# Optimization experiments

Hardware: AMD Instinct MI355X
Metric: run time of the kernel (lower is better)

The kernel has to match this reference:

```python
import jax, jax.numpy as jnp
import numpy as np

N_NODES = 100000


def gcn_conv(x, W, b, src, dst, n_nodes):
    # GCNConv: h = x @ W; add self-loops; symmetric norm; aggregate; + bias
    h = x @ W  # [N, out]
    loop = jnp.arange(n_nodes, dtype=src.dtype)
    s = jnp.concatenate([src, loop])  # source of each message
    d = jnp.concatenate([dst, loop])  # target of each message
    ones = jnp.ones(d.shape[0], dtype=x.dtype)
    deg = jax.ops.segment_sum(ones, d, num_segments=n_nodes)  # in-degree incl. self-loop
    dinv = jnp.where(deg > 0, jax.lax.rsqrt(deg), 0.0)
    norm = dinv[s] * dinv[d]  # [E+N]
    msg = h[s] * norm[:, None]  # gather + scale
    out = jax.ops.segment_sum(msg, d, num_segments=n_nodes)  # scatter-add
    return out + b


def setup_inputs() -> dict:
    key = jax.random.key(0)
    k1, k2, k3, k4, k5 = jax.random.split(key, 5)
    nfeat, nhid, nclass = 128, 128, 40
    x = jax.random.normal(k1, (N_NODES, nfeat), dtype=jnp.float32)
    edge_index = jax.random.randint(k2, (2, 640000), 0, N_NODES, dtype=jnp.int64)
    # Glorot-style init for conv weights, zero bias (PyG defaults)
    W1 = jax.random.normal(k3, (nfeat, nhid), dtype=jnp.float32) * (1.0 / np.sqrt(nfeat))
    b1 = jnp.zeros((nhid,), dtype=jnp.float32)
    W2 = jax.random.normal(k4, (nhid, nclass), dtype=jnp.float32) * (1.0 / np.sqrt(nhid))
    b2 = jnp.zeros((nclass,), dtype=jnp.float32)
    return {"x": x, "edge_index": edge_index, "W1": W1, "b1": b1, "W2": W2, "b2": b2}


def reference(x, edge_index, W1, b1, W2, b2):
    src, dst = edge_index[0], edge_index[1]
    n = x.shape[0]
    # layer 1 + relu (dropout is identity at inference)
    h = gcn_conv(x, W1, b1, src, dst, n)
    h = jax.nn.relu(h)
    # final layer (no activation)
    out = gcn_conv(h, W2, b2, src, dst, n)
    return out
```

## Files before the change

kernel.cpp:

```cpp
#include <hip/hip_runtime.h>
#include <stdint.h>

#define N_NODES 100000
#define NB 782
#define NBP 784
#define BCAP 1536

typedef __attribute__((ext_vector_type(8))) short bf16x8;
typedef __attribute__((ext_vector_type(4))) float f32x4;

__device__ __forceinline__ unsigned short f2bf(float f){
    uint32_t u = __float_as_uint(f);
    uint32_t r = (u + 0x7FFFu + ((u >> 16) & 1u)) >> 16;
    return (unsigned short)r;
}
__device__ __forceinline__ float bf2f(unsigned short h){
    return __uint_as_float(((uint32_t)h) << 16);
}

__global__ void zero_u32(uint32_t* p, int n){
    int i = blockIdx.x * 256 + threadIdx.x;
    if (i < n) p[i] = 0u;
}

__global__ void to_bf16(const float* __restrict__ in, unsigned short* __restrict__ outp, int n4){
    int i = blockIdx.x * 256 + threadIdx.x;
    if (i < n4){
        float4 v = ((const float4*)in)[i];
        ushort4 o = { f2bf(v.x), f2bf(v.y), f2bf(v.z), f2bf(v.w) };
        ((ushort4*)outp)[i] = o;
    }
}

__global__ void transpose_w_frag(const float* __restrict__ W, unsigned short* __restrict__ Wtf,
                                 int NC, int total){
    int i = blockIdx.x * 256 + threadIdx.x;
    if (i < total){
        int j  = i & 7;
        int l  = (i >> 3) & 63;
        int st = (i >> 9) & 3;
        int cb = i >> 11;
        int k   = st * 32 + (l >> 4) * 8 + j;
        int col = cb * 16 + (l & 15);
        float v = (col < NC) ? W[(size_t)k * NC + col] : 0.f;
        Wtf[i] = f2bf(v);
    }
}

__global__ __launch_bounds__(1024) void bucket_hist(const int* __restrict__ dst,
        uint32_t* __restrict__ hist, int E){
    __shared__ uint32_t h[NBP];
    for (int i = threadIdx.x; i < NB; i += 1024) h[i] = 0u;
    __syncthreads();
    int base = blockIdx.x * 12800;
    for (int i = threadIdx.x; i < 12800; i += 1024){
        int e = base + i;
        if (e < E) atomicAdd(&h[(uint32_t)dst[e] >> 7], 1u);
    }
    __syncthreads();
    for (int i = threadIdx.x; i < NB; i += 1024)
        if (h[i]) atomicAdd(&hist[i], h[i]);
}

__global__ void scan_buckets(const uint32_t* __restrict__ hist,
                             uint32_t* __restrict__ base, uint32_t* __restrict__ cur){
    __shared__ uint32_t tmp[1024];
    int t = threadIdx.x;
    for (int j = t; j < 1024; j += 256) tmp[j] = (j < NB) ? hist[j] : 0u;
    __syncthreads();
    for (int off = 1; off < 1024; off <<= 1){
        uint32_t v[4];
        for (int j = 0; j < 4; j++){
            int i = t + j * 256;
            v[j] = (i >= off) ? tmp[i - off] : 0u;
        }
        __syncthreads();
        for (int j = 0; j < 4; j++) tmp[t + j * 256] += v[j];
        __syncthreads();
    }
    for (int j = t; j < NB; j += 256){
        uint32_t v = (j > 0) ? tmp[j - 1] : 0u;
        base[j] = v;
        cur[j] = v;
    }
}

__global__ __launch_bounds__(1024) void bucket_scatter(const int* __restrict__ src,
        const int* __restrict__ dst, uint32_t* __restrict__ cur,
        uint32_t* __restrict__ ebuf, int E){
    __shared__ uint32_t h[NBP];
    __shared__ uint32_t st[NBP];
    for (int i = threadIdx.x; i < NB; i += 1024) h[i] = 0u;
    __syncthreads();
    int base = blockIdx.x * 12800;
    for (int i = threadIdx.x; i < 12800; i += 1024){
        int e = base + i;
        if (e < E) atomicAdd(&h[(uint32_t)dst[e] >> 7], 1u);
    }
    __syncthreads();
    for (int i = threadIdx.x; i < NB; i += 1024){
        uint32_t c = h[i];
        st[i] = c ? atomicAdd(&cur[i], c) : 0u;
        h[i] = 0u;
    }
    __syncthreads();
    for (int i = threadIdx.x; i < 12800; i += 1024){
        int e = base + i;
        if (e < E){
            uint32_t d = (uint32_t)dst[e];
            uint32_t b = d >> 7;
            uint32_t r = atomicAdd(&h[b], 1u);
            ebuf[st[b] + r] = ((d & 127u) << 17) | (uint32_t)src[e];
        }
    }
}

__global__ __launch_bounds__(256) void bucket_csr(const uint32_t* __restrict__ hist,
        const uint32_t* __restrict__ base, const uint32_t* __restrict__ ebuf,
        uint32_t* __restrict__ offs, uint32_t* __restrict__ cnt, float* __restrict__ dinv,
        uint32_t* __restrict__ slot, int N){
    __shared__ uint32_t ebl[BCAP];
    __shared__ uint32_t ncnt[128], loff[128], ncur[128], stmp[128];
    int b = blockIdx.x, t = threadIdx.x;
    uint32_t eb = base[b], ec = hist[b];
    if (ec > BCAP) ec = BCAP;
    for (uint32_t i = t; i < ec; i += 256) ebl[i] = ebuf[eb + i];
    if (t < 128){ ncnt[t] = 0u; ncur[t] = 0u; }
    __syncthreads();
    for (uint32_t i = t; i < ec; i += 256) atomicAdd(&ncnt[ebl[i] >> 17], 1u);
    __syncthreads();
    if (t < 128) stmp[t] = ncnt[t];
    __syncthreads();
    for (int off = 1; off < 128; off <<= 1){
        uint32_t v = 0u;
        if (t < 128 && t >= off) v = stmp[t - off];
        __syncthreads();
        if (t < 128) stmp[t] += v;
        __syncthreads();
    }
    if (t < 128) loff[t] = stmp[t] - ncnt[t];
    __syncthreads();
    int g = b * 128 + t;
    if (t < 128 && g < N){
        offs[g] = eb + loff[t];
        cnt[g]  = ncnt[t];
        dinv[g] = rsqrtf((float)(ncnt[t] + 1u));
    }
    for (uint32_t i = t; i < ec; i += 256){
        uint32_t p  = ebl[i];
        uint32_t ld = p >> 17;
        uint32_t r  = atomicAdd(&ncur[ld], 1u);
        slot[eb + loff[ld] + r] = p & 0x1FFFFu;
    }
}

__global__ __launch_bounds__(256) void agg_bf(const unsigned short* __restrict__ Xh,
        const uint32_t* __restrict__ offs, const uint32_t* __restrict__ cnt,
        const uint32_t* __restrict__ slot, const float* __restrict__ dinv,
        unsigned short* __restrict__ OUT){
    int wgid = blockIdx.x * 4 + (threadIdx.x >> 6);
    int lane = threadIdx.x & 63;
    int h = lane >> 5, l = lane & 31;
    int g = wgid * 2 + h;
    const ushort4* X4 = (const ushort4*)Xh;
    uint32_t o = offs[g], c = cnt[g];
    float ax = 0.f, ay = 0.f, az = 0.f, aw = 0.f;
    #pragma unroll 1
    for (uint32_t base = 0; base < c; base += 32){
        int rem = (int)(c - base); if (rem > 32) rem = 32;
        uint32_t idx = 0u; float ds = 0.f;
        if (l < rem){
            idx = slot[o + base + (uint32_t)l];
            ds = dinv[idx];
        }
        int groups = (rem + 7) >> 3;
        #pragma unroll 1
        for (int gq = 0; gq < groups; gq++){
            int eb = gq * 8;
            ushort4 v[8]; float d[8];
            #pragma unroll
            for (int j = 0; j < 8; j++){
                uint32_t s = (uint32_t)__shfl((int)idx, eb + j, 32);
                d[j] = __shfl(ds, eb + j, 32);
                v[j] = X4[(size_t)s * 32 + l];
            }
            #pragma unroll
            for (int j = 0; j < 8; j++){
                ax += d[j] * bf2f(v[j].x);
                ay += d[j] * bf2f(v[j].y);
                az += d[j] * bf2f(v[j].z);
                aw += d[j] * bf2f(v[j].w);
            }
        }
    }
    float dd = dinv[g];
    ushort4 sv = X4[(size_t)g * 32 + l];
    ushort4 r = { f2bf(dd * (ax + dd * bf2f(sv.x))),
                  f2bf(dd * (ay + dd * bf2f(sv.y))),
                  f2bf(dd * (az + dd * bf2f(sv.z))),
                  f2bf(dd * (aw + dd * bf2f(sv.w))) };
    ((ushort4*)OUT)[(size_t)g * 32 + l] = r;
}

__global__ __launch_bounds__(256) void gemm_mfma_l1(const unsigned short* __restrict__ Xagg,
        const unsigned short* __restrict__ Wtf, const float* __restrict__ bias,
        unsigned short* __restrict__ OUT){
    int tid = threadIdx.x;
    int wid = tid >> 6, l = tid & 63;
    int lm = l & 15, lk = l >> 4;
    int rw = blockIdx.x * 64 + wid * 16;
    int ra = rw + lm; ra = ra < N_NODES ? ra : N_NODES - 1;
    const bf16x8* Wv = (const bf16x8*)Wtf;

    f32x4 acc[8] = {};
    bf16x8 aA, aB, bA[8], bB[8];

    aA = *(const bf16x8*)(Xagg + (size_t)ra * 128 + lk * 8);
    #pragma unroll
    for (int cb = 0; cb < 8; cb++) bA[cb] = Wv[(size_t)(cb * 4 + 0) * 64 + l];

    aB = *(const bf16x8*)(Xagg + (size_t)ra * 128 + 32 + lk * 8);
    #pragma unroll
    for (int cb = 0; cb < 8; cb++) bB[cb] = Wv[(size_t)(cb * 4 + 1) * 64 + l];
    #pragma unroll
    for (int cb = 0; cb < 8; cb++)
        acc[cb] = __builtin_amdgcn_mfma_f32_16x16x32_bf16(aA, bA[cb], acc[cb], 0, 0, 0);

    aA = *(const bf16x8*)(Xagg + (size_t)ra * 128 + 64 + lk * 8);
    #pragma unroll
    for (int cb = 0; cb < 8; cb++) bA[cb] = Wv[(size_t)(cb * 4 + 2) * 64 + l];
    #pragma unroll
    for (int cb = 0; cb < 8; cb++)
        acc[cb] = __builtin_amdgcn_mfma_f32_16x16x32_bf16(aB, bB[cb], acc[cb], 0, 0, 0);

    aB = *(const bf16x8*)(Xagg + (size_t)ra * 128 + 96 + lk * 8);
    #pragma unroll
    for (int cb = 0; cb < 8; cb++) bB[cb] = Wv[(size_t)(cb * 4 + 3) * 64 + l];
    #pragma unroll
    for (int cb = 0; cb < 8; cb++)
        acc[cb] = __builtin_amdgcn_mfma_f32_16x16x32_bf16(aA, bA[cb], acc[cb], 0, 0, 0);

    #pragma unroll
    for (int cb = 0; cb < 8; cb++)
        acc[cb] = __builtin_amdgcn_mfma_f32_16x16x32_bf16(aB, bB[cb], acc[cb], 0, 0, 0);

    #pragma unroll
    for (int cb = 0; cb < 8; cb++){
        int col = cb * 16 + lm;
        float bs = bias[col];
        #pragma unroll
        for (int i = 0; i < 4; i++){
            int row = rw + lk * 4 + i;
            if (row < N_NODES)
                OUT[(size_t)row * 128 + col] = f2bf(fmaxf(acc[cb][i] + bs, 0.f));
        }
    }
}

__global__ __launch_bounds__(256) void gemm_mfma_l2(const unsigned short* __restrict__ Aagg,
        const unsigned short* __restrict__ Wtf, const float* __restrict__ bias,
        float* __restrict__ OUT){
    int tid = threadIdx.x;
    int wid = tid >> 6, l = tid & 63;
    int lm = l & 15, lk = l >> 4;
    int rw = blockIdx.x * 64 + wid * 16;
    int ra = rw + lm; ra = ra < N_NODES ? ra : N_NODES - 1;
    const bf16x8* Wv = (const bf16x8*)Wtf;

    f32x4 acc[3] = {};
    bf16x8 aA, aB, bA[3], bB[3];

    aA = *(const bf16x8*)(Aagg + (size_t)ra * 128 + lk * 8);
    #pragma unroll
    for (int cb = 0; cb < 3; cb++) bA[cb] = Wv[(size_t)(cb * 4 + 0) * 64 + l];

    aB = *(const bf16x8*)(Aagg + (size_t)ra * 128 + 32 + lk * 8);
    #pragma unroll
    for (int cb = 0; cb < 3; cb++) bB[cb] = Wv[(size_t)(cb * 4 + 1) * 64 + l];
    #pragma unroll
    for (int cb = 0; cb < 3; cb++)
        acc[cb] = __builtin_amdgcn_mfma_f32_16x16x32_bf16(aA, bA[cb], acc[cb], 0, 0, 0);

    aA = *(const bf16x8*)(Aagg + (size_t)ra * 128 + 64 + lk * 8);
    #pragma unroll
    for (int cb = 0; cb < 3; cb++) bA[cb] = Wv[(size_t)(cb * 4 + 2) * 64 + l];
    #pragma unroll
    for (int cb = 0; cb < 3; cb++)
        acc[cb] = __builtin_amdgcn_mfma_f32_16x16x32_bf16(aB, bB[cb], acc[cb], 0, 0, 0);

    aB = *(const bf16x8*)(Aagg + (size_t)ra * 128 + 96 + lk * 8);
    #pragma unroll
    for (int cb = 0; cb < 3; cb++) bB[cb] = Wv[(size_t)(cb * 4 + 3) * 64 + l];
    #pragma unroll
    for (int cb = 0; cb < 3; cb++)
        acc[cb] = __builtin_amdgcn_mfma_f32_16x16x32_bf16(aA, bA[cb], acc[cb], 0, 0, 0);

    #pragma unroll
    for (int cb = 0; cb < 3; cb++)
        acc[cb] = __builtin_amdgcn_mfma_f32_16x16x32_bf16(aB, bB[cb], acc[cb], 0, 0, 0);

    #pragma unroll
    for (int cb = 0; cb < 3; cb++){
        int col = cb * 16 + lm;
        if (col < 40){
            float bs = bias[col];
            #pragma unroll
            for (int i = 0; i < 4; i++){
                int row = rw + lk * 4 + i;
                if (row < N_NODES) OUT[(size_t)row * 40 + col] = acc[cb][i] + bs;
            }
        }
    }
}

extern "C" void kernel_launch(void* const* d_in, const int* in_sizes, int n_in,
                              void* d_out, int out_size, void* d_ws, size_t ws_size,
                              hipStream_t stream) {
    const float* x   = (const float*)d_in[0];
    const int*   ei  = (const int*)d_in[1];
    const float* W1  = (const float*)d_in[2];
    const float* b1  = (const float*)d_in[3];
    const float* W2  = (const float*)d_in[4];
    const float* b2  = (const float*)d_in[5];
    float*       out = (float*)d_out;

    const int N = N_NODES;
    const int E = in_sizes[1] / 2;
    const int* src = ei;
    const int* dst = ei + E;

    char* ws = (char*)d_ws;
    size_t o = 0;
    auto alloc = [&](size_t bytes) -> char* {
        char* p = ws + o;
        o += (bytes + 511) & ~(size_t)511;
        return p;
    };
    uint32_t*       hist  = (uint32_t*)alloc((size_t)NBP * 4);
    uint32_t*       bbase = (uint32_t*)alloc((size_t)NBP * 4);
    uint32_t*       bcur  = (uint32_t*)alloc((size_t)NBP * 4);
    uint32_t*       ebuf  = (uint32_t*)alloc((size_t)E * 4);
    uint32_t*       offs  = (uint32_t*)alloc((size_t)N * 4);
    uint32_t*       cnt   = (uint32_t*)alloc((size_t)N * 4);
    uint32_t*       slot  = (uint32_t*)alloc((size_t)E * 4);
    float*          dinv  = (float*)alloc((size_t)N * 4);
    unsigned short* Wtf1  = (unsigned short*)alloc((size_t)8 * 4 * 64 * 8 * 2);
    unsigned short* Wtf2  = (unsigned short*)alloc((size_t)3 * 4 * 64 * 8 * 2);
    unsigned short* Xh    = (unsigned short*)alloc((size_t)N * 128 * 2);
    unsigned short* Xagg  = (unsigned short*)alloc((size_t)N * 128 * 2);
    unsigned short* Ah    = (unsigned short*)alloc((size_t)N * 128 * 2);
    unsigned short* Aagg2 = Xh;

    const int n4 = N * 128 / 4;
    const int nblk_agg = N / 8;
    const int nblk_gemm = (N + 63) / 64;
    const int nblk_edge = (E + 12799) / 12800;

    zero_u32<<<(NBP + 255) / 256, 256, 0, stream>>>(hist, NBP);
    to_bf16<<<(n4 + 255) / 256, 256, 0, stream>>>(x, Xh, n4);
    transpose_w_frag<<<64, 256, 0, stream>>>(W1, Wtf1, 128, 8 * 4 * 64 * 8);
    transpose_w_frag<<<24, 256, 0, stream>>>(W2, Wtf2, 40, 3 * 4 * 64 * 8);
    bucket_hist<<<nblk_edge, 1024, 0, stream>>>(dst, hist, E);
    scan_buckets<<<1, 256, 0, stream>>>(hist, bbase, bcur);
    bucket_scatter<<<nblk_edge, 1024, 0, stream>>>(src, dst, bcur, ebuf, E);
    bucket_csr<<<NB, 256, 0, stream>>>(hist, bbase, ebuf, offs, cnt, dinv, slot, N);

    agg_bf<<<nblk_agg, 256, 0, stream>>>(Xh, offs, cnt, slot, dinv, Xagg);
    gemm_mfma_l1<<<nblk_gemm, 256, 0, stream>>>(Xagg, Wtf1, b1, Ah);

    agg_bf<<<nblk_agg, 256, 0, stream>>>(Ah, offs, cnt, slot, dinv, Aagg2);
    gemm_mfma_l2<<<nblk_gemm, 256, 0, stream>>>(Aagg2, Wtf2, b2, out);
}
```

Measured before the change: 157.1 us.

## Use per-block private histograms, merge setup kernels, add nontemporal stores

Each edge block now writes its own bucket histogram, and a single 1024-thread scan kernel builds per-block start offsets. This removes the zeroing kernel, the global atomics, and the second histogram pass inside the scatter kernel. The two weight-transpose launches are merged into one, and the bf16 conversion handles 8 elements per thread. Nontemporal stores are added to the aggregation and GEMM outputs. Together these cut kernel launches and redundant edge reads, at the cost of a serial per-bucket loop over blocks in the scan.

```diff
diff --git a/kernel.cpp b/kernel.cpp
--- a/kernel.cpp
+++ b/kernel.cpp
@@ -5,9 +5,12 @@
 #define NB 782
 #define NBP 784
 #define BCAP 1536
+#define EPB 12800
 
 typedef __attribute__((ext_vector_type(8))) short bf16x8;
 typedef __attribute__((ext_vector_type(4))) float f32x4;
+typedef __attribute__((ext_vector_type(4))) unsigned short u16x4;
+typedef __attribute__((ext_vector_type(8))) unsigned short u16x8;
 
 __device__ __forceinline__ unsigned short f2bf(float f){
     uint32_t u = __float_as_uint(f);
@@ -18,99 +21,97 @@
     return __uint_as_float(((uint32_t)h) << 16);
 }
 
-__global__ void zero_u32(uint32_t* p, int n){
+__global__ void to_bf16_v8(const float* __restrict__ in, unsigned short* __restrict__ outp, int n8){
     int i = blockIdx.x * 256 + threadIdx.x;
-    if (i < n) p[i] = 0u;
-}
-
-__global__ void to_bf16(const float* __restrict__ in, unsigned short* __restrict__ outp, int n4){
+    if (i < n8){
+        float4 a = ((const float4*)in)[2 * i];
+        float4 b = ((const float4*)in)[2 * i + 1];
+        u16x8 o = { f2bf(a.x), f2bf(a.y), f2bf(a.z), f2bf(a.w),
+                    f2bf(b.x), f2bf(b.y), f2bf(b.z), f2bf(b.w) };
+        __builtin_nontemporal_store(o, &((u16x8*)outp)[i]);
+    }
+}
+
+__global__ void transpose_w_frag2(const float* __restrict__ W1, unsigned short* __restrict__ Wtf1,
+                                  const float* __restrict__ W2, unsigned short* __restrict__ Wtf2){
+    const int T1 = 8 * 4 * 64 * 8;
+    const int T2 = 3 * 4 * 64 * 8;
     int i = blockIdx.x * 256 + threadIdx.x;
-    if (i < n4){
-        float4 v = ((const float4*)in)[i];
-        ushort4 o = { f2bf(v.x), f2bf(v.y), f2bf(v.z), f2bf(v.w) };
-        ((ushort4*)outp)[i] = o;
-    }
-}
-
-__global__ void transpose_w_frag(const float* __restrict__ W, unsigned short* __restrict__ Wtf,
-                                 int NC, int total){
-    int i = blockIdx.x * 256 + threadIdx.x;
-    if (i < total){
-        int j  = i & 7;
-        int l  = (i >> 3) & 63;
-        int st = (i >> 9) & 3;
-        int cb = i >> 11;
-        int k   = st * 32 + (l >> 4) * 8 + j;
-        int col = cb * 16 + (l & 15);
-        float v = (col < NC) ? W[(size_t)k * NC + col] : 0.f;
-        Wtf[i] = f2bf(v);
-    }
-}
-
-__global__ __launch_bounds__(1024) void bucket_hist(const int* __restrict__ dst,
-        uint32_t* __restrict__ hist, int E){
+    if (i < T1){
+        int j = i & 7, l = (i >> 3) & 63, st = (i >> 9) & 3, cb = i >> 11;
+        int k = st * 32 + (l >> 4) * 8 + j, col = cb * 16 + (l & 15);
+        Wtf1[i] = f2bf(W1[(size_t)k * 128 + col]);
+    } else if (i < T1 + T2){
+        int i2 = i - T1;
+        int j = i2 & 7, l = (i2 >> 3) & 63, st = (i2 >> 9) & 3, cb = i2 >> 11;
+        int k = st * 32 + (l >> 4) * 8 + j, col = cb * 16 + (l & 15);
+        Wtf2[i2] = f2bf((col < 40) ? W2[(size_t)k * 40 + col] : 0.f);
+    }
+}
+
+__global__ __launch_bounds__(1024) void bucket_hist_priv(const int* __restrict__ dst,
+        uint32_t* __restrict__ ghist, int E){
     __shared__ uint32_t h[NBP];
-    for (int i = threadIdx.x; i < NB; i += 1024) h[i] = 0u;
-    __syncthreads();
-    int base = blockIdx.x * 12800;
-    for (int i = threadIdx.x; i < 12800; i += 1024){
+    for (int i = threadIdx.x; i < NBP; i += 1024) h[i] = 0u;
+    __syncthreads();
+    int base = blockIdx.x * EPB;
+    for (int i = threadIdx.x; i < EPB; i += 1024){
         int e = base + i;
         if (e < E) atomicAdd(&h[(uint32_t)dst[e] >> 7], 1u);
     }
     __syncthreads();
-    for (int i = threadIdx.x; i < NB; i += 1024)
-        if (h[i]) atomicAdd(&hist[i], h[i]);
-}
-
-__global__ void scan_buckets(const uint32_t* __restrict__ hist,
-                             uint32_t* __restrict__ base, uint32_t* __restrict__ cur){
+    for (int i = threadIdx.x; i < NBP; i += 1024)
+        ghist[blockIdx.x * NBP + i] = h[i];
+}
+
+__global__ __launch_bounds__(1024) void scan_buckets2(const uint32_t* __restrict__ ghist,
+        uint32_t* __restrict__ base, uint32_t* __restrict__ hist,
+        uint32_t* __restrict__ stg, int nblk){
     __shared__ uint32_t tmp[1024];
     int t = threadIdx.x;
-    for (int j = t; j < 1024; j += 256) tmp[j] = (j < NB) ? hist[j] : 0u;
+    uint32_t tot = 0u;
+    if (t < NB){
+        for (int b = 0; b < nblk; b++) tot += ghist[b * NBP + t];
+        hist[t] = tot;
+    }
+    tmp[t] = (t < NB) ? tot : 0u;
     __syncthreads();
     for (int off = 1; off < 1024; off <<= 1){
-        uint32_t v[4];
-        for (int j = 0; j < 4; j++){
-            int i = t + j * 256;
-            v[j] = (i >= off) ? tmp[i - off] : 0u;
-        }
+        uint32_t v = (t >= off) ? tmp[t - off] : 0u;
         __syncthreads();
-        for (int j = 0; j < 4; j++) tmp[t + j * 256] += v[j];
+        tmp[t] += v;
         __syncthreads();
     }
-    for (int j = t; j < NB; j += 256){
-        uint32_t v = (j > 0) ? tmp[j - 1] : 0u;
-        base[j] = v;
-        cur[j] = v;
-    }
-}
-
-__global__ __launch_bounds__(1024) void bucket_scatter(const int* __restrict__ src,
-        const int* __restrict__ dst, uint32_t* __restrict__ cur,
+    if (t < NB){
+        uint32_t ex = tmp[t] - tot;
+        base[t] = ex;
+        uint32_t run = ex;
+        for (int b = 0; b < nblk; b++){
+            stg[b * NBP + t] = run;
+            run += ghist[b * NBP + t];
+        }
+    }
+}
+
+__global__ __launch_bounds__(1024) void bucket_scatter2(const int* __restrict__ src,
+        const int* __restrict__ dst, const uint32_t* __restrict__ stg,
         uint32_t* __restrict__ ebuf, int E){
-    __shared__ uint32_t h[NBP];
-    __shared__ uint32_t st[NBP];
-    for (int i = threadIdx.x; i < NB; i += 1024) h[i] = 0u;
-    __syncthreads();
-    int base = blockIdx.x * 12800;
-    for (int i = threadIdx.x; i < 12800; i += 1024){
-        int e = base + i;
-        if (e < E) atomicAdd(&h[(uint32_t)dst[e] >> 7], 1u);
-    }
-    __syncthreads();
-    for (int i = threadIdx.x; i < NB; i += 1024){
-        uint32_t c = h[i];
-        st[i] = c ? atomicAdd(&cur[i], c) : 0u;
-        h[i] = 0u;
-    }
-    __syncthreads();
-    for (int i = threadIdx.x; i < 12800; i += 1024){
+    __shared__ uint32_t rank[NBP];
+    __shared__ uint32_t stl[NBP];
+    int bl = blockIdx.x;
+    for (int i = threadIdx.x; i < NBP; i += 1024){
+        rank[i] = 0u;
+        stl[i] = stg[bl * NBP + i];
+    }
+    __syncthreads();
+    int base = bl * EPB;
+    for (int i = threadIdx.x; i < EPB; i += 1024){
         int e = base + i;
         if (e < E){
             uint32_t d = (uint32_t)dst[e];
             uint32_t b = d >> 7;
-            uint32_t r = atomicAdd(&h[b], 1u);
-            ebuf[st[b] + r] = ((d & 127u) << 17) | (uint32_t)src[e];
+            uint32_t r = atomicAdd(&rank[b], 1u);
+            ebuf[stl[b] + r] = ((d & 127u) << 17) | (uint32_t)src[e];
         }
     }
 }
@@ -162,7 +163,7 @@
     int lane = threadIdx.x & 63;
     int h = lane >> 5, l = lane & 31;
     int g = wgid * 2 + h;
-    const ushort4* X4 = (const ushort4*)Xh;
+    const u16x4* X4 = (const u16x4*)Xh;
     uint32_t o = offs[g], c = cnt[g];
     float ax = 0.f, ay = 0.f, az = 0.f, aw = 0.f;
     #pragma unroll 1
@@ -177,7 +178,7 @@
         #pragma unroll 1
         for (int gq = 0; gq < groups; gq++){
             int eb = gq * 8;
-            ushort4 v[8]; float d[8];
+            u16x4 v[8]; float d[8];
             #pragma unroll
             for (int j = 0; j < 8; j++){
                 uint32_t s = (uint32_t)__shfl((int)idx, eb + j, 32);
@@ -186,20 +187,20 @@
             }
             #pragma unroll
             for (int j = 0; j < 8; j++){
-                ax += d[j] * bf2f(v[j].x);
-                ay += d[j] * bf2f(v[j].y);
-                az += d[j] * bf2f(v[j].z);
-                aw += d[j] * bf2f(v[j].w);
+                ax += d[j] * bf2f(v[j][0]);
+                ay += d[j] * bf2f(v[j][1]);
+                az += d[j] * bf2f(v[j][2]);
+                aw += d[j] * bf2f(v[j][3]);
             }
         }
     }
     float dd = dinv[g];
-    ushort4 sv = X4[(size_t)g * 32 + l];
-    ushort4 r = { f2bf(dd * (ax + dd * bf2f(sv.x))),
-                  f2bf(dd * (ay + dd * bf2f(sv.y))),
-                  f2bf(dd * (az + dd * bf2f(sv.z))),
-                  f2bf(dd * (aw + dd * bf2f(sv.w))) };
-    ((ushort4*)OUT)[(size_t)g * 32 + l] = r;
+    u16x4 sv = X4[(size_t)g * 32 + l];
+    u16x4 r = { f2bf(dd * (ax + dd * bf2f(sv[0]))),
+                f2bf(dd * (ay + dd * bf2f(sv[1]))),
+                f2bf(dd * (az + dd * bf2f(sv[2]))),
+                f2bf(dd * (aw + dd * bf2f(sv[3]))) };
+    __builtin_nontemporal_store(r, &((u16x4*)OUT)[(size_t)g * 32 + l]);
 }
 
 __global__ __launch_bounds__(256) void gemm_mfma_l1(const unsigned short* __restrict__ Xagg,
@@ -252,7 +253,8 @@
         for (int i = 0; i < 4; i++){
             int row = rw + lk * 4 + i;
             if (row < N_NODES)
-                OUT[(size_t)row * 128 + col] = f2bf(fmaxf(acc[cb][i] + bs, 0.f));
+                __builtin_nontemporal_store(f2bf(fmaxf(acc[cb][i] + bs, 0.f)),
+                                            &OUT[(size_t)row * 128 + col]);
         }
     }
 }
@@ -307,7 +309,8 @@
             #pragma unroll
             for (int i = 0; i < 4; i++){
                 int row = rw + lk * 4 + i;
-                if (row < N_NODES) OUT[(size_t)row * 40 + col] = acc[cb][i] + bs;
+                if (row < N_NODES)
+                    __builtin_nontemporal_store(acc[cb][i] + bs, &OUT[(size_t)row * 40 + col]);
             }
         }
     }
@@ -336,9 +339,11 @@
         o += (bytes + 511) & ~(size_t)511;
         return p;
     };
+    const int nblk_edge = (E + EPB - 1) / EPB;
+    uint32_t*       ghist = (uint32_t*)alloc((size_t)nblk_edge * NBP * 4);
+    uint32_t*       stg   = (uint32_t*)alloc((size_t)nblk_edge * NBP * 4);
     uint32_t*       hist  = (uint32_t*)alloc((size_t)NBP * 4);
     uint32_t*       bbase = (uint32_t*)alloc((size_t)NBP * 4);
-    uint32_t*       bcur  = (uint32_t*)alloc((size_t)NBP * 4);
     uint32_t*       ebuf  = (uint32_t*)alloc((size_t)E * 4);
     uint32_t*       offs  = (uint32_t*)alloc((size_t)N * 4);
     uint32_t*       cnt   = (uint32_t*)alloc((size_t)N * 4);
@@ -351,18 +356,15 @@
     unsigned short* Ah    = (unsigned short*)alloc((size_t)N * 128 * 2);
     unsigned short* Aagg2 = Xh;
 
-    const int n4 = N * 128 / 4;
+    const int n8 = N * 128 / 8;
     const int nblk_agg = N / 8;
     const int nblk_gemm = (N + 63) / 64;
-    const int nblk_edge = (E + 12799) / 12800;
-
-    zero_u32<<<(NBP + 255) / 256, 256, 0, stream>>>(hist, NBP);
-    to_bf16<<<(n4 + 255) / 256, 256, 0, stream>>>(x, Xh, n4);
-    transpose_w_frag<<<64, 256, 0, stream>>>(W1, Wtf1, 128, 8 * 4 * 64 * 8);
-    transpose_w_frag<<<24, 256, 0, stream>>>(W2, Wtf2, 40, 3 * 4 * 64 * 8);
-    bucket_hist<<<nblk_edge, 1024, 0, stream>>>(dst, hist, E);
-    scan_buckets<<<1, 256, 0, stream>>>(hist, bbase, bcur);
-    bucket_scatter<<<nblk_edge, 1024, 0, stream>>>(src, dst, bcur, ebuf, E);
+
+    to_bf16_v8<<<(n8 + 255) / 256, 256, 0, stream>>>(x, Xh, n8);
+    transpose_w_frag2<<<88, 256, 0, stream>>>(W1, Wtf1, W2, Wtf2);
+    bucket_hist_priv<<<nblk_edge, 1024, 0, stream>>>(dst, ghist, E);
+    scan_buckets2<<<1, 1024, 0, stream>>>(ghist, bbase, hist, stg, nblk_edge);
+    bucket_scatter2<<<nblk_edge, 1024, 0, stream>>>(src, dst, stg, ebuf, E);
     bucket_csr<<<NB, 256, 0, stream>>>(hist, bbase, ebuf, offs, cnt, dinv, slot, N);
 
     agg_bf<<<nblk_agg, 256, 0, stream>>>(Xh, offs, cnt, slot, dinv, Xagg);
```

Result: slower. 176.6 us (+12.4%).
